# Performance work log

Hardware: AMD Instinct MI355X
Metric: run time of the kernel (lower is better)

The kernel has to match this reference:

```python
import jax, jax.numpy as jnp
import numpy as np

N_NODES = 50000
N_EDGES = 800000
IN_DIM = 128
OUT_DIM = 64


def setup_inputs() -> dict:
    key = jax.random.key(0)
    k_x, k_r, k_c, k_v, k_w = jax.random.split(key, 5)
    x = jax.random.normal(k_x, (N_NODES, IN_DIM), dtype=jnp.float32)
    edge_row = jax.random.randint(k_r, (N_EDGES,), 0, N_NODES, dtype=jnp.int64)
    edge_col = jax.random.randint(k_c, (N_EDGES,), 0, N_NODES, dtype=jnp.int64)
    edge_val = jax.random.uniform(k_v, (N_EDGES,), dtype=jnp.float32)
    # kaiming_uniform-style init: bound = sqrt(6 / fan_in) with a=sqrt(5) gain folded in torch;
    # exact init values don't affect correctness testing, use a uniform of similar scale.
    bound = float(np.sqrt(6.0 / IN_DIM))
    weight = jax.random.uniform(k_w, (IN_DIM, OUT_DIM), dtype=jnp.float32,
                                minval=-bound, maxval=bound)
    return {"x": x, "edge_row": edge_row, "edge_col": edge_col,
            "edge_val": edge_val, "weight": weight}


def reference(x, edge_row, edge_col, edge_val, weight):
    # dropout p=0.0 -> identity (module default)
    support = x @ weight                              # [N, out_dim] dense GEMM
    # spmm(adj, support): out[i] = sum_e adj_val[e] * support[col[e]] for row[e]==i
    messages = edge_val[:, None] * support[edge_col]  # [E, out_dim] gather
    out = jax.ops.segment_sum(messages, edge_row, num_segments=N_NODES)  # scatter-add
    return jax.nn.relu(out)
```

## Files before the change

### kernel.cpp

```cpp
#include <hip/hip_runtime.h>

#define N_NODES 50000
#define N_EDGES 800000
#define IN_DIM 128
#define OUT_DIM 64

#define GROUP_SHIFT 6
#define GROUP_ROWS 64
#define N_GROUPS 782
#define SLAB 1216
#define CHUNK2 2048
#define FILL_BLOCKS 391

typedef _Float16 h2 __attribute__((ext_vector_type(2)));
typedef _Float16 h4 __attribute__((ext_vector_type(4)));
typedef _Float16 h8 __attribute__((ext_vector_type(8)));
typedef float    f4 __attribute__((ext_vector_type(4)));

#define LDK 136

__global__ __launch_bounds__(256) void fused_gemm_fill(const float* __restrict__ x,
                                                       const float* __restrict__ w,
                                                       const int* __restrict__ erow,
                                                       const int* __restrict__ ecol,
                                                       const float* __restrict__ eval,
                                                       _Float16* __restrict__ support,
                                                       int* __restrict__ gcursor,
                                                       int2* __restrict__ bucket) {
    __shared__ char smem[GROUP_ROWS * LDK * 2 + OUT_DIM * LDK * 2];
    const int tid = threadIdx.x;

    if (blockIdx.x >= FILL_BLOCKS) {
        _Float16* xb = (_Float16*)smem;
        _Float16* wt = (_Float16*)(smem + GROUP_ROWS * LDK * 2);

        {
            const int n_s = tid >> 2;
            const int kp0 = tid & 3;
            #pragma unroll
            for (int it = 0; it < 16; ++it) {
                int kp = kp0 + (it << 2);
                int k  = kp << 1;
                h2 hv = { (_Float16)w[(size_t)k * OUT_DIM + n_s],
                          (_Float16)w[(size_t)(k + 1) * OUT_DIM + n_s] };
                *(h2*)&wt[n_s * LDK + k] = hv;
            }
        }
        const int rowbase = (blockIdx.x - FILL_BLOCKS) * GROUP_ROWS;
        for (int i = tid; i < GROUP_ROWS * (IN_DIM / 4); i += 256) {
            int r  = i >> 5;
            int kq = i & 31;
            int row = rowbase + r;
            float4 v = (row < N_NODES)
                           ? *(const float4*)&x[(size_t)row * IN_DIM + kq * 4]
                           : make_float4(0.f, 0.f, 0.f, 0.f);
            h4 hv = { (_Float16)v.x, (_Float16)v.y, (_Float16)v.z, (_Float16)v.w };
            *(h4*)&xb[r * LDK + kq * 4] = hv;
        }
        __syncthreads();

        const int wave = tid >> 6;
        const int lane = tid & 63;
        const int mrow = lane & 15;
        const int quad = lane >> 4;
        const int m0   = wave * 16;

        f4 acc[4];
        #pragma unroll
        for (int t = 0; t < 4; ++t) acc[t] = (f4){0.f, 0.f, 0.f, 0.f};

        #pragma unroll
        for (int ks = 0; ks < 4; ++ks) {
            int kof = ks * 32 + quad * 8;
            h8 a = *(h8*)&xb[(m0 + mrow) * LDK + kof];
            #pragma unroll
            for (int t = 0; t < 4; ++t) {
                h8 b = *(h8*)&wt[(t * 16 + mrow) * LDK + kof];
                acc[t] = __builtin_amdgcn_mfma_f32_16x16x32_f16(a, b, acc[t], 0, 0, 0);
            }
        }

        #pragma unroll
        for (int t = 0; t < 4; ++t) {
            #pragma unroll
            for (int r = 0; r < 4; ++r) {
                int row = rowbase + m0 + quad * 4 + r;
                if (row < N_NODES)
                    support[(size_t)row * OUT_DIM + t * 16 + mrow] = (_Float16)acc[t][r];
            }
        }
    } else {
        int* lcnt  = (int*)smem;
        int* lbase = lcnt + N_GROUPS;
        for (int i = tid; i < N_GROUPS; i += 256) lcnt[i] = 0;
        __syncthreads();
        const int base = blockIdx.x * CHUNK2;
        #pragma unroll 4
        for (int i = 0; i < CHUNK2 / 256; ++i) {
            int e = base + tid + i * 256;
            if (e < N_EDGES) atomicAdd(&lcnt[erow[e] >> GROUP_SHIFT], 1);
        }
        __syncthreads();
        for (int i = tid; i < N_GROUPS; i += 256) {
            int c = lcnt[i];
            lbase[i] = c ? atomicAdd(&gcursor[i], c) : 0;
            lcnt[i]  = 0;
        }
        __syncthreads();
        #pragma unroll 4
        for (int i = 0; i < CHUNK2 / 256; ++i) {
            int e = base + tid + i * 256;
            if (e < N_EDGES) {
                int r = erow[e];
                int g = r >> GROUP_SHIFT;
                int p = atomicAdd(&lcnt[g], 1);
                bucket[(size_t)g * SLAB + lbase[g] + p] =
                    make_int2(((r & (GROUP_ROWS - 1)) << 16) | ecol[e],
                              __float_as_int(eval[e]));
            }
        }
    }
}

__global__ __launch_bounds__(1024) void reduce_group(const int* __restrict__ gcursor,
                                                     const int2* __restrict__ bucket,
                                                     const _Float16* __restrict__ support,
                                                     float* __restrict__ out) {
    __shared__ int2 ebuf[SLAB];
    __shared__ int2 ebuf2[SLAB];
    __shared__ int  rcnt[GROUP_ROWS];
    __shared__ int  rstart[GROUP_ROWS + 1];
    __shared__ int  rcur[GROUP_ROWS];
    const int grp = blockIdx.x;
    const int cnt = min(gcursor[grp], SLAB);
    const size_t sb = (size_t)grp * SLAB;
    const int tid = threadIdx.x;

    if (tid < GROUP_ROWS) rcnt[tid] = 0;
    __syncthreads();
    for (int j = tid; j < cnt; j += 1024) {
        int2 cv = bucket[sb + j];
        ebuf[j] = cv;
        atomicAdd(&rcnt[cv.x >> 16], 1);
    }
    __syncthreads();
    if (tid < GROUP_ROWS) {
        int v = rcnt[tid];
        int s = v;
        #pragma unroll
        for (int off = 1; off < 64; off <<= 1) {
            int t = __shfl_up(s, off, 64);
            if (tid >= off) s += t;
        }
        rstart[tid] = s - v;
        rcur[tid]   = s - v;
        if (tid == 63) rstart[64] = s;
    }
    __syncthreads();
    for (int j = tid; j < cnt; j += 1024) {
        int2 cv = ebuf[j];
        int rl = cv.x >> 16;
        int p  = atomicAdd(&rcur[rl], 1);
        ebuf2[p] = cv;
    }
    __syncthreads();

    const int g  = tid & 15;
    const int lr = tid >> 4;
    const int row = grp * GROUP_ROWS + lr;
    const int jb = rstart[lr];
    const int je = rstart[lr + 1];
    float4 acc0 = make_float4(0.f, 0.f, 0.f, 0.f);
    float4 acc1 = make_float4(0.f, 0.f, 0.f, 0.f);
    int j = jb;
    for (; j + 1 < je; j += 2) {
        int2 cv0 = ebuf2[j];
        int2 cv1 = ebuf2[j + 1];
        float v0 = __int_as_float(cv0.y);
        float v1 = __int_as_float(cv1.y);
        h4 s0 = *(const h4*)&support[(size_t)(cv0.x & 0xFFFF) * OUT_DIM + g * 4];
        h4 s1 = *(const h4*)&support[(size_t)(cv1.x & 0xFFFF) * OUT_DIM + g * 4];
        acc0.x += v0 * (float)s0[0];
        acc0.y += v0 * (float)s0[1];
        acc0.z += v0 * (float)s0[2];
        acc0.w += v0 * (float)s0[3];
        acc1.x += v1 * (float)s1[0];
        acc1.y += v1 * (float)s1[1];
        acc1.z += v1 * (float)s1[2];
        acc1.w += v1 * (float)s1[3];
    }
    if (j < je) {
        int2 cv = ebuf2[j];
        float v = __int_as_float(cv.y);
        h4 sr = *(const h4*)&support[(size_t)(cv.x & 0xFFFF) * OUT_DIM + g * 4];
        acc0.x += v * (float)sr[0];
        acc0.y += v * (float)sr[1];
        acc0.z += v * (float)sr[2];
        acc0.w += v * (float)sr[3];
    }
    if (row < N_NODES) {
        float4 a;
        a.x = fmaxf(acc0.x + acc1.x, 0.f);
        a.y = fmaxf(acc0.y + acc1.y, 0.f);
        a.z = fmaxf(acc0.z + acc1.z, 0.f);
        a.w = fmaxf(acc0.w + acc1.w, 0.f);
        *(float4*)&out[(size_t)row * OUT_DIM + g * 4] = a;
    }
}

extern "C" void kernel_launch(void* const* d_in, const int* in_sizes, int n_in,
                              void* d_out, int out_size, void* d_ws, size_t ws_size,
                              hipStream_t stream) {
    const float* x    = (const float*)d_in[0];
    const int*   erow = (const int*)  d_in[1];
    const int*   ecol = (const int*)  d_in[2];
    const float* ev   = (const float*)d_in[3];
    const float* w    = (const float*)d_in[4];
    float* out = (float*)d_out;

    char* ws = (char*)d_ws;
    _Float16* support = (_Float16*)ws;
    int*  gcursor = (int*)(ws + 6400000);
    int2* bucket  = (int2*)(ws + 6403200);

    hipMemsetAsync(gcursor, 0, sizeof(int) * N_GROUPS, stream);

    fused_gemm_fill<<<FILL_BLOCKS + N_GROUPS, 256, 0, stream>>>(
        x, w, erow, ecol, ev, support, gcursor, bucket);

    reduce_group<<<N_GROUPS, 1024, 0, stream>>>(gcursor, bucket, support, out);
}
```

Measured before the change: 124.3 us.

## Replace group bucketing with per-row fixed-capacity slabs via global atomics

The two-level group bucketing (shared-memory histogram, global cursor reservation, then an in-block counting sort per 64-row group) is replaced by a direct per-row slab with capacity 64. Each edge does a global atomicAdd on its row counter, and edges are loaded with vectorized int4/float4 reads. The reduce kernel becomes a simple per-row gather with no shared memory or syncs, using 256-thread blocks of 16 rows. The cost is 800k scattered global atomics and a larger, sparser slab footprint, and any row with more than 64 edges silently loses edges (unlikely with mean degree 16).

```diff
diff --git a/kernel.cpp b/kernel.cpp
--- a/kernel.cpp
+++ b/kernel.cpp
@@ -5,12 +5,11 @@
 #define IN_DIM 128
 #define OUT_DIM 64
 
-#define GROUP_SHIFT 6
 #define GROUP_ROWS 64
-#define N_GROUPS 782
-#define SLAB 1216
+#define GEMM_BLOCKS 782
 #define CHUNK2 2048
 #define FILL_BLOCKS 391
+#define ROW_CAP 64
 
 typedef _Float16 h2 __attribute__((ext_vector_type(2)));
 typedef _Float16 h4 __attribute__((ext_vector_type(4)));
@@ -23,10 +22,10 @@
                                                        const float* __restrict__ w,
                                                        const int* __restrict__ erow,
                                                        const int* __restrict__ ecol,
-                                                       const float* __restrict__ eval,
+                                                       const float* __restrict__ ev,
                                                        _Float16* __restrict__ support,
-                                                       int* __restrict__ gcursor,
-                                                       int2* __restrict__ bucket) {
+                                                       int* __restrict__ rowcnt,
+                                                       int2* __restrict__ rowslab) {
     __shared__ char smem[GROUP_ROWS * LDK * 2 + OUT_DIM * LDK * 2];
     const int tid = threadIdx.x;
 
@@ -90,122 +89,80 @@
             }
         }
     } else {
-        int* lcnt  = (int*)smem;
-        int* lbase = lcnt + N_GROUPS;
-        for (int i = tid; i < N_GROUPS; i += 256) lcnt[i] = 0;
-        __syncthreads();
-        const int base = blockIdx.x * CHUNK2;
-        #pragma unroll 4
-        for (int i = 0; i < CHUNK2 / 256; ++i) {
-            int e = base + tid + i * 256;
-            if (e < N_EDGES) atomicAdd(&lcnt[erow[e] >> GROUP_SHIFT], 1);
-        }
-        __syncthreads();
-        for (int i = tid; i < N_GROUPS; i += 256) {
-            int c = lcnt[i];
-            lbase[i] = c ? atomicAdd(&gcursor[i], c) : 0;
-            lcnt[i]  = 0;
-        }
-        __syncthreads();
-        #pragma unroll 4
-        for (int i = 0; i < CHUNK2 / 256; ++i) {
-            int e = base + tid + i * 256;
-            if (e < N_EDGES) {
-                int r = erow[e];
-                int g = r >> GROUP_SHIFT;
-                int p = atomicAdd(&lcnt[g], 1);
-                bucket[(size_t)g * SLAB + lbase[g] + p] =
-                    make_int2(((r & (GROUP_ROWS - 1)) << 16) | ecol[e],
-                              __float_as_int(eval[e]));
+        const int o = blockIdx.x * CHUNK2 + tid * 8;
+        if (o + 8 <= N_EDGES) {
+            int4   ra = *(const int4*)&erow[o];
+            int4   rb = *(const int4*)&erow[o + 4];
+            int4   ca = *(const int4*)&ecol[o];
+            int4   cb = *(const int4*)&ecol[o + 4];
+            float4 va = *(const float4*)&ev[o];
+            float4 vb = *(const float4*)&ev[o + 4];
+            int   rr[8] = { ra.x, ra.y, ra.z, ra.w, rb.x, rb.y, rb.z, rb.w };
+            int   cc[8] = { ca.x, ca.y, ca.z, ca.w, cb.x, cb.y, cb.z, cb.w };
+            float vv[8] = { va.x, va.y, va.z, va.w, vb.x, vb.y, vb.z, vb.w };
+            int pp[8];
+            #pragma unroll
+            for (int k = 0; k < 8; ++k) pp[k] = atomicAdd(&rowcnt[rr[k]], 1);
+            #pragma unroll
+            for (int k = 0; k < 8; ++k)
+                if (pp[k] < ROW_CAP)
+                    rowslab[((size_t)rr[k] << 6) + pp[k]] =
+                        make_int2(cc[k], __float_as_int(vv[k]));
+        } else {
+            #pragma unroll
+            for (int k = 0; k < 8; ++k) {
+                int e = o + k;
+                if (e < N_EDGES) {
+                    int r = erow[e];
+                    int p = atomicAdd(&rowcnt[r], 1);
+                    if (p < ROW_CAP)
+                        rowslab[((size_t)r << 6) + p] =
+                            make_int2(ecol[e], __float_as_int(ev[e]));
+                }
             }
         }
     }
 }
 
-__global__ __launch_bounds__(1024) void reduce_group(const int* __restrict__ gcursor,
-                                                     const int2* __restrict__ bucket,
-                                                     const _Float16* __restrict__ support,
-                                                     float* __restrict__ out) {
-    __shared__ int2 ebuf[SLAB];
-    __shared__ int2 ebuf2[SLAB];
-    __shared__ int  rcnt[GROUP_ROWS];
-    __shared__ int  rstart[GROUP_ROWS + 1];
-    __shared__ int  rcur[GROUP_ROWS];
-    const int grp = blockIdx.x;
-    const int cnt = min(gcursor[grp], SLAB);
-    const size_t sb = (size_t)grp * SLAB;
+__global__ __launch_bounds__(256) void gather_rows(const int* __restrict__ rowcnt,
+                                                   const int2* __restrict__ rowslab,
+                                                   const _Float16* __restrict__ support,
+                                                   float* __restrict__ out) {
     const int tid = threadIdx.x;
+    const int g   = tid & 15;
+    const int lr  = tid >> 4;
+    const int row = blockIdx.x * 16 + lr;
+    const int cnt = min(rowcnt[row], ROW_CAP);
+    const int2* rs = rowslab + ((size_t)row << 6);
+    const _Float16* sp = support + g * 4;
 
-    if (tid < GROUP_ROWS) rcnt[tid] = 0;
-    __syncthreads();
-    for (int j = tid; j < cnt; j += 1024) {
-        int2 cv = bucket[sb + j];
-        ebuf[j] = cv;
-        atomicAdd(&rcnt[cv.x >> 16], 1);
+    float4 a0 = make_float4(0.f, 0.f, 0.f, 0.f);
+    float4 a1 = make_float4(0.f, 0.f, 0.f, 0.f);
+    int j = 0;
+    for (; j + 2 <= cnt; j += 2) {
+        int4 ee = *(const int4*)&rs[j];
+        float v0 = __int_as_float(ee.y);
+        float v1 = __int_as_float(ee.w);
+        h4 s0 = *(const h4*)&sp[(size_t)ee.x * OUT_DIM];
+        h4 s1 = *(const h4*)&sp[(size_t)ee.z * OUT_DIM];
+        a0.x += v0 * (float)s0[0]; a0.y += v0 * (float)s0[1];
+        a0.z += v0 * (float)s0[2]; a0.w += v0 * (float)s0[3];
+        a1.x += v1 * (float)s1[0]; a1.y += v1 * (float)s1[1];
+        a1.z += v1 * (float)s1[2]; a1.w += v1 * (float)s1[3];
     }
-    __syncthreads();
-    if (tid < GROUP_ROWS) {
-        int v = rcnt[tid];
-        int s = v;
-        #pragma unroll
-        for (int off = 1; off < 64; off <<= 1) {
-            int t = __shfl_up(s, off, 64);
-            if (tid >= off) s += t;
-        }
-        rstart[tid] = s - v;
-        rcur[tid]   = s - v;
-        if (tid == 63) rstart[64] = s;
+    if (j < cnt) {
+        int2 e0 = rs[j];
+        float v0 = __int_as_float(e0.y);
+        h4 s0 = *(const h4*)&sp[(size_t)e0.x * OUT_DIM];
+        a0.x += v0 * (float)s0[0]; a0.y += v0 * (float)s0[1];
+        a0.z += v0 * (float)s0[2]; a0.w += v0 * (float)s0[3];
     }
-    __syncthreads();
-    for (int j = tid; j < cnt; j += 1024) {
-        int2 cv = ebuf[j];
-        int rl = cv.x >> 16;
-        int p  = atomicAdd(&rcur[rl], 1);
-        ebuf2[p] = cv;
-    }
-    __syncthreads();
-
-    const int g  = tid & 15;
-    const int lr = tid >> 4;
-    const int row = grp * GROUP_ROWS + lr;
-    const int jb = rstart[lr];
-    const int je = rstart[lr + 1];
-    float4 acc0 = make_float4(0.f, 0.f, 0.f, 0.f);
-    float4 acc1 = make_float4(0.f, 0.f, 0.f, 0.f);
-    int j = jb;
-    for (; j + 1 < je; j += 2) {
-        int2 cv0 = ebuf2[j];
-        int2 cv1 = ebuf2[j + 1];
-        float v0 = __int_as_float(cv0.y);
-        float v1 = __int_as_float(cv1.y);
-        h4 s0 = *(const h4*)&support[(size_t)(cv0.x & 0xFFFF) * OUT_DIM + g * 4];
-        h4 s1 = *(const h4*)&support[(size_t)(cv1.x & 0xFFFF) * OUT_DIM + g * 4];
-        acc0.x += v0 * (float)s0[0];
-        acc0.y += v0 * (float)s0[1];
-        acc0.z += v0 * (float)s0[2];
-        acc0.w += v0 * (float)s0[3];
-        acc1.x += v1 * (float)s1[0];
-        acc1.y += v1 * (float)s1[1];
-        acc1.z += v1 * (float)s1[2];
-        acc1.w += v1 * (float)s1[3];
-    }
-    if (j < je) {
-        int2 cv = ebuf2[j];
-        float v = __int_as_float(cv.y);
-        h4 sr = *(const h4*)&support[(size_t)(cv.x & 0xFFFF) * OUT_DIM + g * 4];
-        acc0.x += v * (float)sr[0];
-        acc0.y += v * (float)sr[1];
-        acc0.z += v * (float)sr[2];
-        acc0.w += v * (float)sr[3];
-    }
-    if (row < N_NODES) {
-        float4 a;
-        a.x = fmaxf(acc0.x + acc1.x, 0.f);
-        a.y = fmaxf(acc0.y + acc1.y, 0.f);
-        a.z = fmaxf(acc0.z + acc1.z, 0.f);
-        a.w = fmaxf(acc0.w + acc1.w, 0.f);
-        *(float4*)&out[(size_t)row * OUT_DIM + g * 4] = a;
-    }
+    float4 r;
+    r.x = fmaxf(a0.x + a1.x, 0.f);
+    r.y = fmaxf(a0.y + a1.y, 0.f);
+    r.z = fmaxf(a0.z + a1.z, 0.f);
+    r.w = fmaxf(a0.w + a1.w, 0.f);
+    *(float4*)&out[(size_t)row * OUT_DIM + g * 4] = r;
 }
 
 extern "C" void kernel_launch(void* const* d_in, const int* in_sizes, int n_in,
@@ -220,13 +177,13 @@
 
     char* ws = (char*)d_ws;
     _Float16* support = (_Float16*)ws;
-    int*  gcursor = (int*)(ws + 6400000);
-    int2* bucket  = (int2*)(ws + 6403200);
+    int*  rowcnt  = (int*)(ws + 6400000);
+    int2* rowslab = (int2*)(ws + 6600000);
 
-    hipMemsetAsync(gcursor, 0, sizeof(int) * N_GROUPS, stream);
+    hipMemsetAsync(rowcnt, 0, sizeof(int) * N_NODES, stream);
 
-    fused_gemm_fill<<<FILL_BLOCKS + N_GROUPS, 256, 0, stream>>>(
-        x, w, erow, ecol, ev, support, gcursor, bucket);
+    fused_gemm_fill<<<FILL_BLOCKS + GEMM_BLOCKS, 256, 0, stream>>>(
+        x, w, erow, ecol, ev, support, rowcnt, rowslab);
 
-    reduce_group<<<N_GROUPS, 1024, 0, stream>>>(gcursor, bucket, support, out);
+    gather_rows<<<N_NODES / 16, 256, 0, stream>>>(rowcnt, rowslab, support, out);
 }
```

New measurement: 147.4 us. +18.6%, slower.

## Replace global-cursor bucketing with per-block fixed-capacity cells plus spill buffer

Applied to the files above, without the earlier changes.

The fill phase no longer does a counting pass and global atomic reservation per group. Each fill block instead writes edges directly into fixed 8-entry cells indexed by (group, block), with overflow going to a small per-group spill area via global atomics, and records per-cell counts as bytes. The reduce kernel gathers from 391 cells plus the spill area into shared memory before the same row sort and accumulation. This removes one pass over erow and most global atomics, at the cost of scattered small reads in the reduce and possible silent drops if cell or spill capacity is exceeded.

```diff
diff --git a/kernel.cpp b/kernel.cpp
--- a/kernel.cpp
+++ b/kernel.cpp
@@ -8,9 +8,11 @@
 #define GROUP_SHIFT 6
 #define GROUP_ROWS 64
 #define N_GROUPS 782
-#define SLAB 1216
 #define CHUNK2 2048
 #define FILL_BLOCKS 391
+#define CELL_CAP 8
+#define SPILL_CAP 64
+#define SLAB 1216
 
 typedef _Float16 h2 __attribute__((ext_vector_type(2)));
 typedef _Float16 h4 __attribute__((ext_vector_type(4)));
@@ -25,7 +27,9 @@
                                                        const int* __restrict__ ecol,
                                                        const float* __restrict__ eval,
                                                        _Float16* __restrict__ support,
-                                                       int* __restrict__ gcursor,
+                                                       int* __restrict__ gspill,
+                                                       unsigned char* __restrict__ cnt8,
+                                                       int2* __restrict__ spill,
                                                        int2* __restrict__ bucket) {
     __shared__ char smem[GROUP_ROWS * LDK * 2 + OUT_DIM * LDK * 2];
     const int tid = threadIdx.x;
@@ -90,40 +94,43 @@
             }
         }
     } else {
-        int* lcnt  = (int*)smem;
-        int* lbase = lcnt + N_GROUPS;
+        int* lcnt = (int*)smem;
         for (int i = tid; i < N_GROUPS; i += 256) lcnt[i] = 0;
         __syncthreads();
-        const int base = blockIdx.x * CHUNK2;
-        #pragma unroll 4
-        for (int i = 0; i < CHUNK2 / 256; ++i) {
-            int e = base + tid + i * 256;
-            if (e < N_EDGES) atomicAdd(&lcnt[erow[e] >> GROUP_SHIFT], 1);
-        }
-        __syncthreads();
-        for (int i = tid; i < N_GROUPS; i += 256) {
-            int c = lcnt[i];
-            lbase[i] = c ? atomicAdd(&gcursor[i], c) : 0;
-            lcnt[i]  = 0;
-        }
-        __syncthreads();
-        #pragma unroll 4
+        const int base  = blockIdx.x * CHUNK2;
+        const int cbase = blockIdx.x;
+        #pragma unroll
         for (int i = 0; i < CHUNK2 / 256; ++i) {
             int e = base + tid + i * 256;
             if (e < N_EDGES) {
                 int r = erow[e];
+                int c = ecol[e];
+                float v = eval[e];
                 int g = r >> GROUP_SHIFT;
+                int payload = ((r & (GROUP_ROWS - 1)) << 16) | c;
                 int p = atomicAdd(&lcnt[g], 1);
-                bucket[(size_t)g * SLAB + lbase[g] + p] =
-                    make_int2(((r & (GROUP_ROWS - 1)) << 16) | ecol[e],
-                              __float_as_int(eval[e]));
-            }
-        }
+                if (p < CELL_CAP) {
+                    bucket[((size_t)g * FILL_BLOCKS + cbase) * CELL_CAP + p] =
+                        make_int2(payload, __float_as_int(v));
+                } else {
+                    int sp = atomicAdd(&gspill[g], 1);
+                    if (sp < SPILL_CAP)
+                        spill[(size_t)g * SPILL_CAP + sp] =
+                            make_int2(payload, __float_as_int(v));
+                }
+            }
+        }
+        __syncthreads();
+        for (int i = tid; i < N_GROUPS; i += 256)
+            cnt8[(size_t)cbase * N_GROUPS + i] =
+                (unsigned char)min(lcnt[i], CELL_CAP);
     }
 }
 
-__global__ __launch_bounds__(1024) void reduce_group(const int* __restrict__ gcursor,
+__global__ __launch_bounds__(1024) void reduce_group(const unsigned char* __restrict__ cnt8,
+                                                     const int* __restrict__ gspill,
                                                      const int2* __restrict__ bucket,
+                                                     const int2* __restrict__ spill,
                                                      const _Float16* __restrict__ support,
                                                      float* __restrict__ out) {
     __shared__ int2 ebuf[SLAB];
@@ -131,19 +138,39 @@
     __shared__ int  rcnt[GROUP_ROWS];
     __shared__ int  rstart[GROUP_ROWS + 1];
     __shared__ int  rcur[GROUP_ROWS];
+    __shared__ int  tot;
     const int grp = blockIdx.x;
-    const int cnt = min(gcursor[grp], SLAB);
-    const size_t sb = (size_t)grp * SLAB;
     const int tid = threadIdx.x;
 
     if (tid < GROUP_ROWS) rcnt[tid] = 0;
-    __syncthreads();
-    for (int j = tid; j < cnt; j += 1024) {
-        int2 cv = bucket[sb + j];
-        ebuf[j] = cv;
-        atomicAdd(&rcnt[cv.x >> 16], 1);
-    }
-    __syncthreads();
+    if (tid == 0) tot = 0;
+    __syncthreads();
+
+    if (tid < FILL_BLOCKS) {
+        int k = cnt8[(size_t)tid * N_GROUPS + grp];
+        if (k) {
+            int p = atomicAdd(&tot, k);
+            const int2* cell = &bucket[((size_t)grp * FILL_BLOCKS + tid) * CELL_CAP];
+            #pragma unroll 4
+            for (int j = 0; j < k; ++j) {
+                int2 cv = cell[j];
+                if (p + j < SLAB) ebuf[p + j] = cv;
+                atomicAdd(&rcnt[cv.x >> 16], 1);
+            }
+        }
+    } else if (tid < FILL_BLOCKS + SPILL_CAP) {
+        int t  = tid - FILL_BLOCKS;
+        int cs = min(gspill[grp], SPILL_CAP);
+        if (t < cs) {
+            int2 cv = spill[(size_t)grp * SPILL_CAP + t];
+            int p = atomicAdd(&tot, 1);
+            if (p < SLAB) ebuf[p] = cv;
+            atomicAdd(&rcnt[cv.x >> 16], 1);
+        }
+    }
+    __syncthreads();
+    const int cnt = min(tot, SLAB);
+
     if (tid < GROUP_ROWS) {
         int v = rcnt[tid];
         int s = v;
@@ -161,15 +188,15 @@
         int2 cv = ebuf[j];
         int rl = cv.x >> 16;
         int p  = atomicAdd(&rcur[rl], 1);
-        ebuf2[p] = cv;
+        if (p < SLAB) ebuf2[p] = cv;
     }
     __syncthreads();
 
     const int g  = tid & 15;
     const int lr = tid >> 4;
     const int row = grp * GROUP_ROWS + lr;
-    const int jb = rstart[lr];
-    const int je = rstart[lr + 1];
+    const int jb = min(rstart[lr], SLAB);
+    const int je = min(rstart[lr + 1], SLAB);
     float4 acc0 = make_float4(0.f, 0.f, 0.f, 0.f);
     float4 acc1 = make_float4(0.f, 0.f, 0.f, 0.f);
     int j = jb;
@@ -219,14 +246,17 @@
     float* out = (float*)d_out;
 
     char* ws = (char*)d_ws;
-    _Float16* support = (_Float16*)ws;
-    int*  gcursor = (int*)(ws + 6400000);
-    int2* bucket  = (int2*)(ws + 6403200);
-
-    hipMemsetAsync(gcursor, 0, sizeof(int) * N_GROUPS, stream);
+    _Float16*      support = (_Float16*)ws;
+    int*           gspill  = (int*)(ws + 6400000);
+    unsigned char* cnt8    = (unsigned char*)(ws + 6403200);
+    int2*          spill   = (int2*)(ws + 6709504);
+    int2*          bucket  = (int2*)(ws + 7109888);
+
+    hipMemsetAsync(gspill, 0, sizeof(int) * N_GROUPS, stream);
 
     fused_gemm_fill<<<FILL_BLOCKS + N_GROUPS, 256, 0, stream>>>(
-        x, w, erow, ecol, ev, support, gcursor, bucket);
-
-    reduce_group<<<N_GROUPS, 1024, 0, stream>>>(gcursor, bucket, support, out);
+        x, w, erow, ecol, ev, support, gspill, cnt8, spill, bucket);
+
+    reduce_group<<<N_GROUPS, 1024, 0, stream>>>(cnt8, gspill, bucket, spill,
+                                                support, out);
 }
```

New measurement: 130.5 us. +5.0%, slower.

## Replace global atomic bucket cursors with deterministic count-scan-fill and unroll gather by four

Applied to the files above, without the earlier changes.

Edge bucketing is split into a per-block group histogram kernel, a column-wise scan kernel that computes each block's base offset per group, and a fill pass that reads those precomputed offsets. This removes the global atomicAdd on group cursors and the memset. The fill pass still uses a shared-memory atomic for the slot within a block, so bucket order is not fully deterministic. The reduce loop is also unrolled to four independent gathers and accumulators to raise memory-level parallelism. In exchange it adds two extra kernel launches and an extra pass over edge_row, and the fill no longer overlaps counting with the GEMM blocks.

```diff
diff --git a/kernel.cpp b/kernel.cpp
--- a/kernel.cpp
+++ b/kernel.cpp
@@ -8,9 +8,9 @@
 #define GROUP_SHIFT 6
 #define GROUP_ROWS 64
 #define N_GROUPS 782
-#define SLAB 1216
 #define CHUNK2 2048
 #define FILL_BLOCKS 391
+#define SLAB 1216
 
 typedef _Float16 h2 __attribute__((ext_vector_type(2)));
 typedef _Float16 h4 __attribute__((ext_vector_type(4)));
@@ -18,6 +18,48 @@
 typedef float    f4 __attribute__((ext_vector_type(4)));
 
 #define LDK 136
+
+__global__ __launch_bounds__(256) void count_edges(const int* __restrict__ erow,
+                                                   unsigned short* __restrict__ cnt16) {
+    __shared__ int lcnt[N_GROUPS];
+    const int tid = threadIdx.x;
+    for (int i = tid; i < N_GROUPS; i += 256) lcnt[i] = 0;
+    __syncthreads();
+    const int base = blockIdx.x * CHUNK2;
+    #pragma unroll
+    for (int i = 0; i < CHUNK2 / 256; ++i) {
+        int e = base + tid + i * 256;
+        if (e < N_EDGES) atomicAdd(&lcnt[erow[e] >> GROUP_SHIFT], 1);
+    }
+    __syncthreads();
+    for (int i = tid; i < N_GROUPS; i += 256)
+        cnt16[(size_t)blockIdx.x * N_GROUPS + i] = (unsigned short)lcnt[i];
+}
+
+__global__ __launch_bounds__(256) void scan_bases(const unsigned short* __restrict__ cnt16,
+                                                  unsigned short* __restrict__ rbase,
+                                                  int* __restrict__ gtot) {
+    const int sub = threadIdx.x >> 5;
+    const int l   = threadIdx.x & 31;
+    const int g   = blockIdx.x * 8 + sub;
+    if (g >= N_GROUPS) return;
+    const int b0 = l * 13;
+    const int b1 = min(b0 + 13, FILL_BLOCKS);
+    int s = 0;
+    for (int b = b0; b < b1; ++b) s += cnt16[(size_t)b * N_GROUPS + g];
+    int incl = s;
+    #pragma unroll
+    for (int off = 1; off < 32; off <<= 1) {
+        int t = __shfl_up(incl, off, 32);
+        if (l >= off) incl += t;
+    }
+    int run = incl - s;
+    for (int b = b0; b < b1; ++b) {
+        rbase[(size_t)b * N_GROUPS + g] = (unsigned short)run;
+        run += cnt16[(size_t)b * N_GROUPS + g];
+    }
+    if (l == 31) gtot[g] = incl;
+}
 
 __global__ __launch_bounds__(256) void fused_gemm_fill(const float* __restrict__ x,
                                                        const float* __restrict__ w,
@@ -25,7 +67,7 @@
                                                        const int* __restrict__ ecol,
                                                        const float* __restrict__ eval,
                                                        _Float16* __restrict__ support,
-                                                       int* __restrict__ gcursor,
+                                                       const unsigned short* __restrict__ rbase,
                                                        int2* __restrict__ bucket) {
     __shared__ char smem[GROUP_ROWS * LDK * 2 + OUT_DIM * LDK * 2];
     const int tid = threadIdx.x;
@@ -90,39 +132,31 @@
             }
         }
     } else {
-        int* lcnt  = (int*)smem;
-        int* lbase = lcnt + N_GROUPS;
+        int* lcnt = (int*)smem;
         for (int i = tid; i < N_GROUPS; i += 256) lcnt[i] = 0;
         __syncthreads();
-        const int base = blockIdx.x * CHUNK2;
-        #pragma unroll 4
-        for (int i = 0; i < CHUNK2 / 256; ++i) {
-            int e = base + tid + i * 256;
-            if (e < N_EDGES) atomicAdd(&lcnt[erow[e] >> GROUP_SHIFT], 1);
-        }
-        __syncthreads();
-        for (int i = tid; i < N_GROUPS; i += 256) {
-            int c = lcnt[i];
-            lbase[i] = c ? atomicAdd(&gcursor[i], c) : 0;
-            lcnt[i]  = 0;
-        }
-        __syncthreads();
-        #pragma unroll 4
+        const int b    = blockIdx.x;
+        const int base = b * CHUNK2;
+        #pragma unroll
         for (int i = 0; i < CHUNK2 / 256; ++i) {
             int e = base + tid + i * 256;
             if (e < N_EDGES) {
                 int r = erow[e];
+                int c = ecol[e];
+                float v = eval[e];
                 int g = r >> GROUP_SHIFT;
                 int p = atomicAdd(&lcnt[g], 1);
-                bucket[(size_t)g * SLAB + lbase[g] + p] =
-                    make_int2(((r & (GROUP_ROWS - 1)) << 16) | ecol[e],
-                              __float_as_int(eval[e]));
-            }
-        }
-    }
-}
-
-__global__ __launch_bounds__(1024) void reduce_group(const int* __restrict__ gcursor,
+                int pos = (int)rbase[(size_t)b * N_GROUPS + g] + p;
+                if (pos < SLAB)
+                    bucket[(size_t)g * SLAB + pos] =
+                        make_int2(((r & (GROUP_ROWS - 1)) << 16) | c,
+                                  __float_as_int(v));
+            }
+        }
+    }
+}
+
+__global__ __launch_bounds__(1024) void reduce_group(const int* __restrict__ gtot,
                                                      const int2* __restrict__ bucket,
                                                      const _Float16* __restrict__ support,
                                                      float* __restrict__ out) {
@@ -132,7 +166,7 @@
     __shared__ int  rstart[GROUP_ROWS + 1];
     __shared__ int  rcur[GROUP_ROWS];
     const int grp = blockIdx.x;
-    const int cnt = min(gcursor[grp], SLAB);
+    const int cnt = min(gtot[grp], SLAB);
     const size_t sb = (size_t)grp * SLAB;
     const int tid = threadIdx.x;
 
@@ -170,40 +204,46 @@
     const int row = grp * GROUP_ROWS + lr;
     const int jb = rstart[lr];
     const int je = rstart[lr + 1];
-    float4 acc0 = make_float4(0.f, 0.f, 0.f, 0.f);
-    float4 acc1 = make_float4(0.f, 0.f, 0.f, 0.f);
+    float4 A0 = make_float4(0.f, 0.f, 0.f, 0.f);
+    float4 A1 = make_float4(0.f, 0.f, 0.f, 0.f);
+    float4 A2 = make_float4(0.f, 0.f, 0.f, 0.f);
+    float4 A3 = make_float4(0.f, 0.f, 0.f, 0.f);
     int j = jb;
-    for (; j + 1 < je; j += 2) {
-        int2 cv0 = ebuf2[j];
-        int2 cv1 = ebuf2[j + 1];
-        float v0 = __int_as_float(cv0.y);
-        float v1 = __int_as_float(cv1.y);
-        h4 s0 = *(const h4*)&support[(size_t)(cv0.x & 0xFFFF) * OUT_DIM + g * 4];
-        h4 s1 = *(const h4*)&support[(size_t)(cv1.x & 0xFFFF) * OUT_DIM + g * 4];
-        acc0.x += v0 * (float)s0[0];
-        acc0.y += v0 * (float)s0[1];
-        acc0.z += v0 * (float)s0[2];
-        acc0.w += v0 * (float)s0[3];
-        acc1.x += v1 * (float)s1[0];
-        acc1.y += v1 * (float)s1[1];
-        acc1.z += v1 * (float)s1[2];
-        acc1.w += v1 * (float)s1[3];
-    }
-    if (j < je) {
+    for (; j + 4 <= je; j += 4) {
+        int2 c0 = ebuf2[j];
+        int2 c1 = ebuf2[j + 1];
+        int2 c2 = ebuf2[j + 2];
+        int2 c3 = ebuf2[j + 3];
+        h4 s0 = *(const h4*)&support[(size_t)(c0.x & 0xFFFF) * OUT_DIM + g * 4];
+        h4 s1 = *(const h4*)&support[(size_t)(c1.x & 0xFFFF) * OUT_DIM + g * 4];
+        h4 s2 = *(const h4*)&support[(size_t)(c2.x & 0xFFFF) * OUT_DIM + g * 4];
+        h4 s3 = *(const h4*)&support[(size_t)(c3.x & 0xFFFF) * OUT_DIM + g * 4];
+        float v0 = __int_as_float(c0.y);
+        float v1 = __int_as_float(c1.y);
+        float v2 = __int_as_float(c2.y);
+        float v3 = __int_as_float(c3.y);
+        A0.x += v0 * (float)s0[0]; A0.y += v0 * (float)s0[1];
+        A0.z += v0 * (float)s0[2]; A0.w += v0 * (float)s0[3];
+        A1.x += v1 * (float)s1[0]; A1.y += v1 * (float)s1[1];
+        A1.z += v1 * (float)s1[2]; A1.w += v1 * (float)s1[3];
+        A2.x += v2 * (float)s2[0]; A2.y += v2 * (float)s2[1];
+        A2.z += v2 * (float)s2[2]; A2.w += v2 * (float)s2[3];
+        A3.x += v3 * (float)s3[0]; A3.y += v3 * (float)s3[1];
+        A3.z += v3 * (float)s3[2]; A3.w += v3 * (float)s3[3];
+    }
+    for (; j < je; ++j) {
         int2 cv = ebuf2[j];
         float v = __int_as_float(cv.y);
         h4 sr = *(const h4*)&support[(size_t)(cv.x & 0xFFFF) * OUT_DIM + g * 4];
-        acc0.x += v * (float)sr[0];
-        acc0.y += v * (float)sr[1];
-        acc0.z += v * (float)sr[2];
-        acc0.w += v * (float)sr[3];
+        A0.x += v * (float)sr[0]; A0.y += v * (float)sr[1];
+        A0.z += v * (float)sr[2]; A0.w += v * (float)sr[3];
     }
     if (row < N_NODES) {
         float4 a;
-        a.x = fmaxf(acc0.x + acc1.x, 0.f);
-        a.y = fmaxf(acc0.y + acc1.y, 0.f);
-        a.z = fmaxf(acc0.z + acc1.z, 0.f);
-        a.w = fmaxf(acc0.w + acc1.w, 0.f);
+        a.x = fmaxf(A0.x + A1.x + A2.x + A3.x, 0.f);
+        a.y = fmaxf(A0.y + A1.y + A2.y + A3.y, 0.f);
+        a.z = fmaxf(A0.z + A1.z + A2.z + A3.z, 0.f);
+        a.w = fmaxf(A0.w + A1.w + A2.w + A3.w, 0.f);
         *(float4*)&out[(size_t)row * OUT_DIM + g * 4] = a;
     }
 }
@@ -219,14 +259,15 @@
     float* out = (float*)d_out;
 
     char* ws = (char*)d_ws;
-    _Float16* support = (_Float16*)ws;
-    int*  gcursor = (int*)(ws + 6400000);
-    int2* bucket  = (int2*)(ws + 6403200);
-
-    hipMemsetAsync(gcursor, 0, sizeof(int) * N_GROUPS, stream);
-
+    _Float16*       support = (_Float16*)ws;
+    unsigned short* cnt16   = (unsigned short*)(ws + 6400000);
+    unsigned short* rbase   = (unsigned short*)(ws + 7011584);
+    int*            gtot    = (int*)(ws + 7623168);
+    int2*           bucket  = (int2*)(ws + 7626496);
+
+    count_edges<<<FILL_BLOCKS, 256, 0, stream>>>(erow, cnt16);
+    scan_bases<<<(N_GROUPS + 7) / 8, 256, 0, stream>>>(cnt16, rbase, gtot);
     fused_gemm_fill<<<FILL_BLOCKS + N_GROUPS, 256, 0, stream>>>(
-        x, w, erow, ecol, ev, support, gcursor, bucket);
-
-    reduce_group<<<N_GROUPS, 1024, 0, stream>>>(gcursor, bucket, support, out);
-}
+        x, w, erow, ecol, ev, support, rbase, bucket);
+    reduce_group<<<N_GROUPS, 1024, 0, stream>>>(gtot, bucket, support, out);
+}
```

Result: slower. 130.0 us (+4.6%).
